# Performance work log

Measured on AMD Instinct MI355X. Metric: run time of the kernel, lower is better.

## Reference

```python
import jax, jax.numpy as jnp
import numpy as np

EPS = 1e-20
K = 3  # kernel_size and max_pool_size


def _patches3(x):
    # x: [B,C,Hp,Wp] already padded by 1; returns [B,C,9,Hp-2,Wp-2] in torch-unfold kernel order
    H, W = x.shape[2] - 2, x.shape[3] - 2
    return jnp.stack([x[:, :, i:i + H, j:j + W] for i in range(3) for j in range(3)], axis=2)


def _pad1(x):
    return jnp.pad(x, ((0, 0), (0, 0), (1, 1), (1, 1)))


def _conv(x, w):
    return jax.lax.conv_general_dilated(x, w, (1, 1), ((1, 1), (1, 1)),
                                        dimension_numbers=('NCHW', 'OIHW', 'NCHW'))


def _prepare_weights(w_channel_d, w_spatial_d, w_pow_s, w_prop_s, w_channel_s, w_spatial_s):
    sp = jax.nn.softplus
    wcd, wsd, wcs, wss = sp(w_channel_d), sp(w_spatial_d), sp(w_channel_s), sp(w_spatial_s)
    wps = jax.nn.sigmoid(w_prop_s)
    wpow = sp(w_pow_s)
    # symmetric: mirror the first k//2 columns (k=3 -> 1 column)
    wsd = jnp.concatenate([wsd, wsd[:, :, :K // 2][:, :, ::-1]], axis=2)  # [i,3,3]
    wss = jnp.concatenate([wss, wss[:, :, :K // 2][:, :, ::-1]], axis=2)
    wcd = wcd / jnp.sum(wcd, axis=1, keepdims=True)
    wsd = wsd / jnp.sum(wsd, axis=(1, 2), keepdims=True)
    wcs = wcs / jnp.sum(wcs, axis=1, keepdims=True)
    wss = wss / jnp.sum(wss, axis=(1, 2), keepdims=True)
    w_conv_d = jnp.einsum('oi,ihw->oihw', wcd, wsd).reshape(wcd.shape[0], wcd.shape[1], K * K)  # [o,i,9]
    w_conv_s = jnp.einsum('oi,ihw->oihw', wcs, wss)  # [o,i,3,3]
    return w_conv_d, wps, wpow, w_conv_s


def setup_inputs() -> dict:
    key = jax.random.key(0)
    ks = jax.random.split(key, 9)
    B, C, H, W = 4, 1, 768, 768
    return {
        'x': jax.random.uniform(ks[0], (2 * B, C, H, W), dtype=jnp.float32),
        'scs': jax.random.uniform(ks[1], (B, C, H, W), dtype=jnp.float32),
        'cs': jax.random.uniform(ks[2], (B, C, H, W), dtype=jnp.float32),
        'w_channel_d': jnp.ones((1, 1), jnp.float32),
        'w_spatial_d': jax.random.uniform(ks[3], (1, 3, 2), dtype=jnp.float32),
        'w_pow_s': jax.random.uniform(ks[4], (1,), dtype=jnp.float32),
        'w_prop_s': jax.random.uniform(ks[5], (1,), dtype=jnp.float32),
        'w_channel_s': jnp.ones((1, 1), jnp.float32),
        'w_spatial_s': jax.random.uniform(ks[6], (1, 3, 2), dtype=jnp.float32),
    }


def reference(x, scs, cs, w_channel_d, w_spatial_d, w_pow_s, w_prop_s, w_channel_s, w_spatial_s):
    w_conv_d, wps, wpow, w_conv_s = _prepare_weights(
        w_channel_d, w_spatial_d, w_pow_s, w_prop_s, w_channel_s, w_spatial_s)
    B = cs.shape[0]
    dcd, cd = x[:B], x[B:]

    # stop-gradient pooling branch (torch uses .detach())
    dcd_sg, cd_sg = jax.lax.stop_gradient(dcd), jax.lax.stop_gradient(cd)
    d_pad = _pad1(dcd_sg / (cd_sg + EPS))
    cd_pad = _pad1(cd_sg)

    dp = _patches3(d_pad)   # [B,C,9,H,W]
    cp = _patches3(cd_pad)  # [B,C,9,H,W]
    j_max = jnp.argmax(dp * cp, axis=2)            # argmax of d*cd in each 3x3 window
    j_min = jnp.argmax(cp / (dp + EPS), axis=2)    # argmax of cd/d

    def _gather(p, j):
        return jnp.take_along_axis(p, j[:, :, None], axis=2)[:, :, 0]

    d_jmax, d_jmin = _gather(dp, j_max), _gather(dp, j_min)
    cd_jmax, cd_jmin = _gather(cp, j_max), _gather(cp, j_min)

    wpow_b = wpow.reshape(1, -1, 1, 1)  # n_in == 1
    wps_b = wps.reshape(1, -1, 1, 1)
    s_new = ((d_jmin + EPS) / (d_jmax + EPS)) ** wpow_b
    cs_new = cd_jmax * cd_jmin

    cs_out = _conv(cs * wps_b + cs_new * (1.0 - wps_b), w_conv_s)
    scs_out = _conv(scs * wps_b + s_new * cs_new * (1.0 - wps_b), w_conv_s)
    s = scs_out / (cs_out + EPS)

    # data-dependent per-pixel weights w_s: [B,C,9,H,W], center fixed to 1
    w_s = _patches3(_pad1(s)) * s[:, :, None]
    w_s = w_s.at[:, :, 4].set(1.0)

    ud = _patches3(_pad1(dcd))  # [B,C,9,H,W]
    uc = _patches3(_pad1(cd))
    num_d = jnp.einsum('bikhw,oik->bohw', ud * w_s, w_conv_d)
    num_c = jnp.einsum('bikhw,oik->bohw', uc * w_s, w_conv_d)
    den = jnp.einsum('bikhw,oik->bohw', w_s, w_conv_d) + EPS
    x_out = (jnp.stack((num_d, num_c), axis=1) / den[:, None]).reshape(2 * B, *s.shape[1:])
    return x_out, scs_out, cs_out
```

## Files before the change

### kernel.cpp

```cpp
#include <hip/hip_runtime.h>
#include <hip/hip_fp16.h>

#define EPSF 1e-20f

constexpr int Hh = 768, Ww = 768, Bb = 4;
constexpr int PLANE = Hh * Ww;
constexpr int TSX = 32, TSY = 24;
constexpr int R3Y = TSY + 6, R3X = TSX + 6;
constexpr int R2Y = TSY + 4, R2X = TSX + 4;
constexpr int R1Y = TSY + 2, R1X = TSX + 2;

struct Smem {
    float2 s_qc[R3Y][R3X];
    float2 s_t[R2Y][R2X];
    float2 cbuf[R1Y][R1X];
    __half s_s[R1Y][R1X];
    float  sw[20];
    float  swraw[18];
};

template<bool EDGE>
__device__ __forceinline__
void tile_body(Smem& sm, int b, int ty0, int tx0,
               const float* __restrict__ x, const float* __restrict__ scs,
               const float* __restrict__ cs, float* __restrict__ out) {
    auto& s_qc = sm.s_qc; auto& s_t = sm.s_t; auto& s_s = sm.s_s;
    auto& cbuf = sm.cbuf; auto& sw = sm.sw;

    const int tid = threadIdx.x;
    const float* dcd = x + b * PLANE;
    const float* cd  = x + (Bb + b) * PLANE;

    for (int it = tid; it < R3Y * 10; it += 256) {
        int row = it / 10, seg = it - row * 10;
        int gy = ty0 - 3 + row;
        int gxb = tx0 - 4 + seg * 4;
        float4 vd4, vc4;
        if constexpr (!EDGE) {
            vd4 = *(const float4*)(dcd + gy * Ww + gxb);
            vc4 = *(const float4*)(cd  + gy * Ww + gxb);
        } else {
            vd4 = make_float4(0.f, 0.f, 0.f, 0.f);
            vc4 = vd4;
            if ((unsigned)gy < (unsigned)Hh) {
                bool safe = (seg > 0 && seg < 9) || (seg == 0 ? (tx0 > 0) : (tx0 + TSX < Ww));
                if (safe) {
                    vd4 = *(const float4*)(dcd + gy * Ww + gxb);
                    vc4 = *(const float4*)(cd  + gy * Ww + gxb);
                } else {
                    if ((unsigned)(gxb + 0) < (unsigned)Ww) { vd4.x = dcd[gy*Ww+gxb+0]; vc4.x = cd[gy*Ww+gxb+0]; }
                    if ((unsigned)(gxb + 1) < (unsigned)Ww) { vd4.y = dcd[gy*Ww+gxb+1]; vc4.y = cd[gy*Ww+gxb+1]; }
                    if ((unsigned)(gxb + 2) < (unsigned)Ww) { vd4.z = dcd[gy*Ww+gxb+2]; vc4.z = cd[gy*Ww+gxb+2]; }
                    if ((unsigned)(gxb + 3) < (unsigned)Ww) { vd4.w = dcd[gy*Ww+gxb+3]; vc4.w = cd[gy*Ww+gxb+3]; }
                }
            }
        }
        int lxb = seg * 4 - 1;
        if ((unsigned)(lxb + 0) < (unsigned)R3X) s_qc[row][lxb + 0] = make_float2(vd4.x / (vc4.x + EPSF), vc4.x);
        if ((unsigned)(lxb + 1) < (unsigned)R3X) s_qc[row][lxb + 1] = make_float2(vd4.y / (vc4.y + EPSF), vc4.y);
        if ((unsigned)(lxb + 2) < (unsigned)R3X) s_qc[row][lxb + 2] = make_float2(vd4.z / (vc4.z + EPSF), vc4.z);
        if ((unsigned)(lxb + 3) < (unsigned)R3X) s_qc[row][lxb + 3] = make_float2(vd4.w / (vc4.w + EPSF), vc4.w);
    }

    const int xB = tid % R2X;
    const int tyB = tid / R2X;
    const int yb0 = tyB * 4;
    float pcs[4], pscs[4];
    if (tyB < 7) {
        int gx = tx0 - 2 + xB;
        if constexpr (!EDGE) {
            #pragma unroll
            for (int j = 0; j < 4; ++j) {
                int idx = b * PLANE + (ty0 - 2 + yb0 + j) * Ww + gx;
                pcs[j]  = cs[idx];
                pscs[j] = scs[idx];
            }
        } else {
            bool colok = (unsigned)gx < (unsigned)Ww;
            #pragma unroll
            for (int j = 0; j < 4; ++j) {
                int gy = ty0 - 2 + yb0 + j;
                bool ok = colok && (unsigned)gy < (unsigned)Hh;
                int idx = ok ? (b * PLANE + gy * Ww + gx) : 0;
                pcs[j]  = ok ? cs[idx]  : 0.f;
                pscs[j] = ok ? scs[idx] : 0.f;
            }
        }
    }
    __syncthreads();

    const float wps  = sw[18];
    const float wpow = sw[19];
    const float onemw = 1.f - wps;

    if (tyB < 7) {
        float ma[3], md[3], mc[3];
        float nv[3], nq[3];
#define HROW_B(rr, slot) { \
        float2 q0 = s_qc[rr][xB]; float2 q1 = s_qc[rr][xB + 1]; float2 q2 = s_qc[rr][xB + 2]; \
        float a0 = q0.x * q0.y, a1 = q1.x * q1.y, a2 = q2.x * q2.y; \
        float A = a0, D = q0.x, C = q0.y; \
        if (a1 > A) { A = a1; D = q1.x; C = q1.y; } \
        if (a2 > A) { A = a2; D = q2.x; C = q2.y; } \
        ma[slot] = A; md[slot] = D; mc[slot] = C; \
        float V = q0.y, Q = q0.x + EPSF; \
        float e1 = q1.x + EPSF, e2 = q2.x + EPSF; \
        if (q1.y * Q > V * e1) { V = q1.y; Q = e1; } \
        if (q2.y * Q > V * e2) { V = q2.y; Q = e2; } \
        nv[slot] = V; nq[slot] = Q; }
        HROW_B(yb0 + 0, 0)
        HROW_B(yb0 + 1, 1)
        #pragma unroll
        for (int j = 0; j < 4; ++j) {
            const int sl2 = (j + 2) % 3, s0 = j % 3, s1 = (j + 1) % 3;
            HROW_B(yb0 + j + 2, sl2)
            float A = ma[s0], D = md[s0], C = mc[s0];
            if (ma[s1]  > A) { A = ma[s1];  D = md[s1];  C = mc[s1];  }
            if (ma[sl2] > A) { A = ma[sl2]; D = md[sl2]; C = mc[sl2]; }
            float V = nv[s0], Q = nq[s0];
            if (nv[s1]  * Q > V * nq[s1])  { V = nv[s1];  Q = nq[s1];  }
            if (nv[sl2] * Q > V * nq[sl2]) { V = nv[sl2]; Q = nq[sl2]; }
            const int yb = yb0 + j;
            bool in_img;
            if constexpr (!EDGE) in_img = true;
            else {
                const int gy = ty0 - 2 + yb, gx = tx0 - 2 + xB;
                in_img = (unsigned)gy < (unsigned)Hh && (unsigned)gx < (unsigned)Ww;
            }
            float tc = 0.f, ts = 0.f;
            if (in_img) {
                float s_new = __builtin_amdgcn_exp2f(wpow *
                    (__builtin_amdgcn_logf(Q) - __builtin_amdgcn_logf(D + EPSF)));
                float cs_new = C * V;
                tc = pcs[j]  * wps + cs_new * onemw;
                ts = pscs[j] * wps + s_new * cs_new * onemw;
            }
            s_t[yb][xB] = make_float2(tc, ts);
        }
    }
    __syncthreads();

    const int xC = tid % R1X;
    const int tyC = tid / R1X;
    const int yc0 = tyC * 4;
    if (tyC < 7) {
        const float wa0 = sw[9],  wb0 = sw[10];
        const float wa1 = sw[12], wb1 = sw[13];
        const float wa2 = sw[15], wb2 = sw[16];
        float2 u[3], tm[3];
#define HROW_C(rr, slot) { \
        float2 t0 = s_t[rr][xC]; float2 t1 = s_t[rr][xC + 1]; float2 t2 = s_t[rr][xC + 2]; \
        u[slot] = make_float2(t0.x + t2.x, t0.y + t2.y); tm[slot] = t1; }
        HROW_C(yc0 + 0, 0)
        HROW_C(yc0 + 1, 1)
        #pragma unroll
        for (int j = 0; j < 4; ++j) {
            const int yc = yc0 + j;
            if (yc < R1Y) {
                const int sl2 = (j + 2) % 3, s0 = j % 3, s1 = (j + 1) % 3;
                HROW_C(yc + 2, sl2)
                float accC = wa0 * u[s0].x + wb0 * tm[s0].x
                           + wa1 * u[s1].x + wb1 * tm[s1].x
                           + wa2 * u[sl2].x + wb2 * tm[sl2].x;
                float accS = wa0 * u[s0].y + wb0 * tm[s0].y
                           + wa1 * u[s1].y + wb1 * tm[s1].y
                           + wa2 * u[sl2].y + wb2 * tm[sl2].y;
                bool in_img;
                if constexpr (!EDGE) in_img = true;
                else {
                    const int gy = ty0 - 1 + yc, gx = tx0 - 1 + xC;
                    in_img = (unsigned)gy < (unsigned)Hh && (unsigned)gx < (unsigned)Ww;
                }
                s_s[yc][xC] = __float2half(
                    in_img ? (accS * __builtin_amdgcn_rcpf(accC + EPSF)) : 0.f);
                cbuf[yc][xC] = make_float2(accC, accS);
            }
        }
    }
    __syncthreads();

    {
        const int xD = tid & 31, tyD = tid >> 5;
        const int yd0 = tyD * 3;
        float wdk[9];
        #pragma unroll
        for (int k = 0; k < 9; ++k) wdk[k] = sw[k];
        float  srw[3][3];
        float2 qrw[3][3];
#define HROW_D(rr, slot) { \
        srw[slot][0] = __half2float(s_s[rr][xD]); \
        srw[slot][1] = __half2float(s_s[rr][xD + 1]); \
        srw[slot][2] = __half2float(s_s[rr][xD + 2]); \
        qrw[slot][0] = s_qc[rr + 2][xD + 2]; qrw[slot][1] = s_qc[rr + 2][xD + 3]; qrw[slot][2] = s_qc[rr + 2][xD + 4]; }
        HROW_D(yd0 + 0, 0)
        HROW_D(yd0 + 1, 1)
#define TAP_F(slot, kk, cc2) { \
        float t = wdk[kk] * srw[slot][cc2]; \
        float2 q = qrw[slot][cc2]; \
        dn_p += t; \
        nd_p = fmaf(t, q.x * (q.y + EPSF), nd_p); \
        nc_p = fmaf(t, q.y, nc_p); }
        #pragma unroll
        for (int j = 0; j < 3; ++j) {
            const int sl2 = (j + 2) % 3, s0 = j % 3, s1 = (j + 1) % 3;
            HROW_D(yd0 + j + 2, sl2)
            float sc = srw[s1][1];
            float nd_p = 0.f, nc_p = 0.f, dn_p = 0.f;
            TAP_F(s0, 0, 0) TAP_F(s0, 1, 1) TAP_F(s0, 2, 2)
            TAP_F(s1, 3, 0)                 TAP_F(s1, 5, 2)
            TAP_F(sl2, 6, 0) TAP_F(sl2, 7, 1) TAP_F(sl2, 8, 2)
            const float w4 = wdk[4];
            float2 q4 = qrw[s1][1];
            float d4 = q4.x * (q4.y + EPSF);
            float den = fmaf(sc, dn_p, w4) + EPSF;
            float nd  = fmaf(sc, nd_p, w4 * d4);
            float nc  = fmaf(sc, nc_p, w4 * q4.y);
            float rinv = __builtin_amdgcn_rcpf(den);
            const int iy = yd0 + j;
            int idx = (ty0 + iy) * Ww + (tx0 + xD);
            float2 cv = cbuf[iy + 1][xD + 1];
            out[(2 * b)     * PLANE + idx] = nd * rinv;
            out[(2 * b + 1) * PLANE + idx] = nc * rinv;
            out[(8 + b)     * PLANE + idx] = cv.y;
            out[(12 + b)    * PLANE + idx] = cv.x;
        }
    }
}

__global__ __launch_bounds__(256)
void fused_all(const float* __restrict__ x, const float* __restrict__ scs,
               const float* __restrict__ cs,
               const float* __restrict__ w_sp_d, const float* __restrict__ w_sp_s,
               const float* __restrict__ w_pow_s, const float* __restrict__ w_prop_s,
               float* __restrict__ out) {
    __shared__ Smem sm;
    const int tid = threadIdx.x;

    if (tid < 9) {
        int r = tid / 3, c = tid - r * 3;
        int cc = (c == 2) ? 0 : c;
        sm.swraw[tid]     = log1pf(expf(w_sp_d[r * 2 + cc]));
        sm.swraw[9 + tid] = log1pf(expf(w_sp_s[r * 2 + cc]));
    }
    if (tid == 9)  sm.sw[18] = 1.f / (1.f + expf(-w_prop_s[0]));
    if (tid == 10) sm.sw[19] = log1pf(expf(w_pow_s[0]));
    if (tid < 9) {
        float sum_d = 0.f, sum_s = 0.f;
        #pragma unroll
        for (int k = 0; k < 9; ++k) { sum_d += sm.swraw[k]; sum_s += sm.swraw[9 + k]; }
        sm.sw[tid]     = sm.swraw[tid]     / sum_d;
        sm.sw[9 + tid] = sm.swraw[9 + tid] / sum_s;
    }

    const int orig = blockIdx.x;
    const int swz  = (orig & 7) * 192 + (orig >> 3);
    const int b    = swz / 384;
    const int rem  = swz - b * 384;
    const int tyP  = rem / 24;
    const int txT  = rem % 24;
    const int ty1  = 2 * tyP, ty2 = 2 * tyP + 1;
    const bool colEdge = (txT == 0) || (txT == 23);
    const bool e1 = colEdge || (ty1 == 0);
    const bool e2 = colEdge || (ty2 == 31);

    if (e1) tile_body<true >(sm, b, ty1 * TSY, txT * TSX, x, scs, cs, out);
    else    tile_body<false>(sm, b, ty1 * TSY, txT * TSX, x, scs, cs, out);
    __syncthreads();
    if (e2) tile_body<true >(sm, b, ty2 * TSY, txT * TSX, x, scs, cs, out);
    else    tile_body<false>(sm, b, ty2 * TSY, txT * TSX, x, scs, cs, out);
}

extern "C" void kernel_launch(void* const* d_in, const int* in_sizes, int n_in,
                              void* d_out, int out_size, void* d_ws, size_t ws_size,
                              hipStream_t stream) {
    const float* x        = (const float*)d_in[0];
    const float* scs      = (const float*)d_in[1];
    const float* cs       = (const float*)d_in[2];
    const float* w_sp_d   = (const float*)d_in[4];
    const float* w_pow_s  = (const float*)d_in[5];
    const float* w_prop_s = (const float*)d_in[6];
    const float* w_sp_s   = (const float*)d_in[8];
    float* out  = (float*)d_out;

    fused_all<<<dim3(1536), 256, 0, stream>>>(x, scs, cs, w_sp_d, w_sp_s,
                                              w_pow_s, w_prop_s, out);
}
```

Measured before the change: 29.17 us.

## Prefetch next tile's input into registers during current tile's final stage

The first 256 float4 loads of the x halo for each tile are now issued into registers ahead of time. For the first tile they are issued before the weight-prep code, and for the second tile they are issued after the last barrier of the first tile, so their latency overlaps with the output stage. This hides global-load latency across the two tiles each block processes. It adds register pressure from the extra float4 pairs and duplicates some guarded load logic.

Measured after the change: 33.10 us. 13.5% more time.

```diff
diff --git a/kernel.cpp b/kernel.cpp
--- a/kernel.cpp
+++ b/kernel.cpp
@@ -19,11 +19,63 @@
     float  swraw[18];
 };
 
+__device__ __forceinline__
+void load_A_guarded(int it, int ty0, int tx0,
+                    const float* __restrict__ dcd, const float* __restrict__ cd,
+                    float4& vd4, float4& vc4) {
+    int row = it / 10, seg = it - row * 10;
+    int gy = ty0 - 3 + row;
+    int gxb = tx0 - 4 + seg * 4;
+    vd4 = make_float4(0.f, 0.f, 0.f, 0.f);
+    vc4 = vd4;
+    if ((unsigned)gy < (unsigned)Hh) {
+        bool safe = (seg > 0 && seg < 9) || (seg == 0 ? (tx0 > 0) : (tx0 + TSX < Ww));
+        if (safe) {
+            vd4 = *(const float4*)(dcd + gy * Ww + gxb);
+            vc4 = *(const float4*)(cd  + gy * Ww + gxb);
+        } else {
+            if ((unsigned)(gxb + 0) < (unsigned)Ww) { vd4.x = dcd[gy*Ww+gxb+0]; vc4.x = cd[gy*Ww+gxb+0]; }
+            if ((unsigned)(gxb + 1) < (unsigned)Ww) { vd4.y = dcd[gy*Ww+gxb+1]; vc4.y = cd[gy*Ww+gxb+1]; }
+            if ((unsigned)(gxb + 2) < (unsigned)Ww) { vd4.z = dcd[gy*Ww+gxb+2]; vc4.z = cd[gy*Ww+gxb+2]; }
+            if ((unsigned)(gxb + 3) < (unsigned)Ww) { vd4.w = dcd[gy*Ww+gxb+3]; vc4.w = cd[gy*Ww+gxb+3]; }
+        }
+    }
+}
+
 template<bool EDGE>
+__device__ __forceinline__
+void load_A(int it, int ty0, int tx0,
+            const float* __restrict__ dcd, const float* __restrict__ cd,
+            float4& vd4, float4& vc4) {
+    if constexpr (!EDGE) {
+        int row = it / 10, seg = it - row * 10;
+        int gy = ty0 - 3 + row;
+        int gxb = tx0 - 4 + seg * 4;
+        vd4 = *(const float4*)(dcd + gy * Ww + gxb);
+        vc4 = *(const float4*)(cd  + gy * Ww + gxb);
+    } else {
+        load_A_guarded(it, ty0, tx0, dcd, cd, vd4, vc4);
+    }
+}
+
+__device__ __forceinline__
+void store_A(Smem& sm, int it, float4 vd4, float4 vc4) {
+    int row = it / 10, seg = it - row * 10;
+    int lxb = seg * 4 - 1;
+    if ((unsigned)(lxb + 0) < (unsigned)R3X) sm.s_qc[row][lxb + 0] = make_float2(vd4.x / (vc4.x + EPSF), vc4.x);
+    if ((unsigned)(lxb + 1) < (unsigned)R3X) sm.s_qc[row][lxb + 1] = make_float2(vd4.y / (vc4.y + EPSF), vc4.y);
+    if ((unsigned)(lxb + 2) < (unsigned)R3X) sm.s_qc[row][lxb + 2] = make_float2(vd4.z / (vc4.z + EPSF), vc4.z);
+    if ((unsigned)(lxb + 3) < (unsigned)R3X) sm.s_qc[row][lxb + 3] = make_float2(vd4.w / (vc4.w + EPSF), vc4.w);
+}
+
+template<bool EDGE, bool ISSUE_NEXT>
 __device__ __forceinline__
 void tile_body(Smem& sm, int b, int ty0, int tx0,
                const float* __restrict__ x, const float* __restrict__ scs,
-               const float* __restrict__ cs, float* __restrict__ out) {
+               const float* __restrict__ cs, float* __restrict__ out,
+               float4 pvd, float4 pvc,
+               int nty0, int ntx0,
+               float4& npvd, float4& npvc) {
     auto& s_qc = sm.s_qc; auto& s_t = sm.s_t; auto& s_s = sm.s_s;
     auto& cbuf = sm.cbuf; auto& sw = sm.sw;
 
@@ -31,35 +83,11 @@
     const float* dcd = x + b * PLANE;
     const float* cd  = x + (Bb + b) * PLANE;
 
-    for (int it = tid; it < R3Y * 10; it += 256) {
-        int row = it / 10, seg = it - row * 10;
-        int gy = ty0 - 3 + row;
-        int gxb = tx0 - 4 + seg * 4;
+    store_A(sm, tid, pvd, pvc);
+    if (tid < R3Y * 10 - 256) {
         float4 vd4, vc4;
-        if constexpr (!EDGE) {
-            vd4 = *(const float4*)(dcd + gy * Ww + gxb);
-            vc4 = *(const float4*)(cd  + gy * Ww + gxb);
-        } else {
-            vd4 = make_float4(0.f, 0.f, 0.f, 0.f);
-            vc4 = vd4;
-            if ((unsigned)gy < (unsigned)Hh) {
-                bool safe = (seg > 0 && seg < 9) || (seg == 0 ? (tx0 > 0) : (tx0 + TSX < Ww));
-                if (safe) {
-                    vd4 = *(const float4*)(dcd + gy * Ww + gxb);
-                    vc4 = *(const float4*)(cd  + gy * Ww + gxb);
-                } else {
-                    if ((unsigned)(gxb + 0) < (unsigned)Ww) { vd4.x = dcd[gy*Ww+gxb+0]; vc4.x = cd[gy*Ww+gxb+0]; }
-                    if ((unsigned)(gxb + 1) < (unsigned)Ww) { vd4.y = dcd[gy*Ww+gxb+1]; vc4.y = cd[gy*Ww+gxb+1]; }
-                    if ((unsigned)(gxb + 2) < (unsigned)Ww) { vd4.z = dcd[gy*Ww+gxb+2]; vc4.z = cd[gy*Ww+gxb+2]; }
-                    if ((unsigned)(gxb + 3) < (unsigned)Ww) { vd4.w = dcd[gy*Ww+gxb+3]; vc4.w = cd[gy*Ww+gxb+3]; }
-                }
-            }
-        }
-        int lxb = seg * 4 - 1;
-        if ((unsigned)(lxb + 0) < (unsigned)R3X) s_qc[row][lxb + 0] = make_float2(vd4.x / (vc4.x + EPSF), vc4.x);
-        if ((unsigned)(lxb + 1) < (unsigned)R3X) s_qc[row][lxb + 1] = make_float2(vd4.y / (vc4.y + EPSF), vc4.y);
-        if ((unsigned)(lxb + 2) < (unsigned)R3X) s_qc[row][lxb + 2] = make_float2(vd4.z / (vc4.z + EPSF), vc4.z);
-        if ((unsigned)(lxb + 3) < (unsigned)R3X) s_qc[row][lxb + 3] = make_float2(vd4.w / (vc4.w + EPSF), vc4.w);
+        load_A<EDGE>(tid + 256, ty0, tx0, dcd, cd, vd4, vc4);
+        store_A(sm, tid + 256, vd4, vc4);
     }
 
     const int xB = tid % R2X;
@@ -178,6 +206,10 @@
         }
     }
     __syncthreads();
+
+    if constexpr (ISSUE_NEXT) {
+        load_A_guarded(tid, nty0, ntx0, dcd, cd, npvd, npvc);
+    }
 
     {
         const int xD = tid & 31, tyD = tid >> 5;
@@ -236,22 +268,6 @@
     __shared__ Smem sm;
     const int tid = threadIdx.x;
 
-    if (tid < 9) {
-        int r = tid / 3, c = tid - r * 3;
-        int cc = (c == 2) ? 0 : c;
-        sm.swraw[tid]     = log1pf(expf(w_sp_d[r * 2 + cc]));
-        sm.swraw[9 + tid] = log1pf(expf(w_sp_s[r * 2 + cc]));
-    }
-    if (tid == 9)  sm.sw[18] = 1.f / (1.f + expf(-w_prop_s[0]));
-    if (tid == 10) sm.sw[19] = log1pf(expf(w_pow_s[0]));
-    if (tid < 9) {
-        float sum_d = 0.f, sum_s = 0.f;
-        #pragma unroll
-        for (int k = 0; k < 9; ++k) { sum_d += sm.swraw[k]; sum_s += sm.swraw[9 + k]; }
-        sm.sw[tid]     = sm.swraw[tid]     / sum_d;
-        sm.sw[9 + tid] = sm.swraw[9 + tid] / sum_s;
-    }
-
     const int orig = blockIdx.x;
     const int swz  = (orig & 7) * 192 + (orig >> 3);
     const int b    = swz / 384;
@@ -259,15 +275,43 @@
     const int tyP  = rem / 24;
     const int txT  = rem % 24;
     const int ty1  = 2 * tyP, ty2 = 2 * tyP + 1;
+    const int tx0  = txT * TSX;
     const bool colEdge = (txT == 0) || (txT == 23);
     const bool e1 = colEdge || (ty1 == 0);
     const bool e2 = colEdge || (ty2 == 31);
 
-    if (e1) tile_body<true >(sm, b, ty1 * TSY, txT * TSX, x, scs, cs, out);
-    else    tile_body<false>(sm, b, ty1 * TSY, txT * TSX, x, scs, cs, out);
+    const float* dcd = x + b * PLANE;
+    const float* cd  = x + (Bb + b) * PLANE;
+    float4 p1d, p1c;
+    load_A_guarded(tid, ty1 * TSY, tx0, dcd, cd, p1d, p1c);
+
+    if (tid < 9) {
+        int r = tid / 3, c = tid - r * 3;
+        int cc = (c == 2) ? 0 : c;
+        sm.swraw[tid]     = log1pf(expf(w_sp_d[r * 2 + cc]));
+        sm.swraw[9 + tid] = log1pf(expf(w_sp_s[r * 2 + cc]));
+    }
+    if (tid == 9)  sm.sw[18] = 1.f / (1.f + expf(-w_prop_s[0]));
+    if (tid == 10) sm.sw[19] = log1pf(expf(w_pow_s[0]));
+    if (tid < 9) {
+        float sum_d = 0.f, sum_s = 0.f;
+        #pragma unroll
+        for (int k = 0; k < 9; ++k) { sum_d += sm.swraw[k]; sum_s += sm.swraw[9 + k]; }
+        sm.sw[tid]     = sm.swraw[tid]     / sum_d;
+        sm.sw[9 + tid] = sm.swraw[9 + tid] / sum_s;
+    }
+
+    float4 p2d, p2c;
+    if (e1) tile_body<true , true>(sm, b, ty1 * TSY, tx0, x, scs, cs, out,
+                                   p1d, p1c, ty2 * TSY, tx0, p2d, p2c);
+    else    tile_body<false, true>(sm, b, ty1 * TSY, tx0, x, scs, cs, out,
+                                   p1d, p1c, ty2 * TSY, tx0, p2d, p2c);
     __syncthreads();
-    if (e2) tile_body<true >(sm, b, ty2 * TSY, txT * TSX, x, scs, cs, out);
-    else    tile_body<false>(sm, b, ty2 * TSY, txT * TSX, x, scs, cs, out);
+    float4 du0, du1;
+    if (e2) tile_body<true , false>(sm, b, ty2 * TSY, tx0, x, scs, cs, out,
+                                    p2d, p2c, 0, 0, du0, du1);
+    else    tile_body<false, false>(sm, b, ty2 * TSY, tx0, x, scs, cs, out,
+                                    p2d, p2c, 0, 0, du0, du1);
 }
 
 extern "C" void kernel_launch(void* const* d_in, const int* in_sizes, int n_in,
```
